# Performance work log

Hardware: AMD Instinct MI355X
Metric: run time of the kernel (lower is better)

## Reference

```python
import jax, jax.numpy as jnp
import numpy as np

B, S, WIDTH, M = 2, 240, 128, 20
PAD = 16


def setup_inputs() -> dict:
    key = jax.random.key(0)
    ks = jax.random.split(key, 10)
    scale = 1.0 / (WIDTH * WIDTH)
    inp = {
        "x": jax.random.normal(ks[0], (B, S, S, 3), jnp.float32),
        "fc0_w": jax.random.normal(ks[1], (5, WIDTH), jnp.float32) * 0.1,
        "fc0_b": jnp.zeros((WIDTH,), jnp.float32),
        # 5 spectral layers, complex weights stored as [..., 2] = (real, imag)
        "spec_w1": jax.random.uniform(ks[2], (5, WIDTH, WIDTH, M, M, 2), jnp.float32) * scale,
        "spec_w2": jax.random.uniform(ks[3], (5, WIDTH, WIDTH, M, M, 2), jnp.float32) * scale,
        # 5 residual 1x1 convs
        "w_w": jax.random.normal(ks[4], (5, WIDTH, WIDTH), jnp.float32) / np.sqrt(WIDTH),
        "w_b": jnp.zeros((5, WIDTH), jnp.float32),
        "fc1_w": jax.random.normal(ks[5], (WIDTH, WIDTH), jnp.float32) / np.sqrt(WIDTH),
        "fc1_b": jnp.zeros((WIDTH,), jnp.float32),
        # 4 heads (u, v, p, T): width->64->1
        "head1_w": jax.random.normal(ks[6], (4, WIDTH, 64), jnp.float32) / np.sqrt(WIDTH),
        "head1_b": jnp.zeros((4, 64), jnp.float32),
        "head2_w": jax.random.normal(ks[7], (4, 64, 1), jnp.float32) / 8.0,
        "head2_b": jnp.zeros((4, 1), jnp.float32),
    }
    return inp


def _spectral_conv(h, w1, w2):
    # h: (B, C, H, W) real; w1, w2: (C_in, C_out, M, M) complex64
    Hh, Ww = h.shape[-2], h.shape[-1]
    ft = jnp.fft.rfft2(h)  # (B, C, H, W//2+1)
    o1 = jnp.einsum('bixy,ioxy->boxy', ft[:, :, :M, :M], w1)
    o2 = jnp.einsum('bixy,ioxy->boxy', ft[:, :, -M:, :M], w2)
    out_ft = jnp.zeros((h.shape[0], w1.shape[1], Hh, Ww // 2 + 1), jnp.complex64)
    out_ft = out_ft.at[:, :, :M, :M].set(o1).at[:, :, -M:, :M].set(o2)
    return jnp.fft.irfft2(out_ft, s=(Hh, Ww))


def reference(x, fc0_w, fc0_b, spec_w1, spec_w2, w_w, w_b, fc1_w, fc1_b,
              head1_w, head1_b, head2_w, head2_b):
    Bn, sx, sy = x.shape[0], x.shape[1], x.shape[2]
    gx = jnp.broadcast_to(jnp.linspace(0.0, 1.0, sx, dtype=x.dtype)[None, :, None, None], (Bn, sx, sy, 1))
    gy = jnp.broadcast_to(jnp.linspace(0.0, 1.0, sy, dtype=x.dtype)[None, None, :, None], (Bn, sx, sy, 1))
    x1 = jnp.concatenate([x, gx, gy], axis=-1)          # (B, S, S, 5)
    h = x1 @ fc0_w + fc0_b                              # lift -> (B, S, S, width)
    h = jnp.transpose(h, (0, 3, 1, 2))                  # (B, width, S, S)
    h = jnp.pad(h, ((0, 0), (0, 0), (0, PAD), (0, PAD)))
    c1 = spec_w1[..., 0] + 1j * spec_w1[..., 1]
    c2 = spec_w2[..., 0] + 1j * spec_w2[..., 1]
    for i in range(5):
        s = _spectral_conv(h, c1[i], c2[i])
        lin = jnp.einsum('bchw,oc->bohw', h, w_w[i]) + w_b[i][None, :, None, None]
        h = s + lin
        if i < 4:
            h = jax.nn.gelu(h, approximate=False)
    h = h[..., :-PAD, :-PAD]
    h = jnp.transpose(h, (0, 2, 3, 1))                  # (B, S, S, width)
    h = jax.nn.gelu(h @ fc1_w + fc1_b, approximate=False)
    h1 = jax.nn.gelu(jnp.einsum('bhwc,kcd->kbhwd', h, head1_w)
                     + head1_b[:, None, None, None, :], approximate=False)
    out = jnp.einsum('kbhwd,kdo->kbhwo', h1, head2_w) + head2_b[:, None, None, None, :]
    return (out[0], out[1], out[2], out[3])  # u, v, p, T each (B, S, S, 1)
```

## Files before the change

kernel.cpp:

```cpp
#include <hip/hip_runtime.h>
#include <math.h>


#define SZ_H   (2ull*256*256*128)
#define O_HA   0ull
#define O_HB   (O_HA + SZ_H)
#define O_G    (O_HB + SZ_H)
#define SZ_G   (2ull*256*20*128*2)
#define O_FTT  (O_G + SZ_G)
#define SZ_FT  (2ull*40*20*128*2)
#define O_OFT  (O_FTT + SZ_FT)
#define O_EY   (O_OFT + SZ_FT)
#define SZ_EY  (256ull*20*2)
#define O_EX   (O_EY + SZ_EY)
#define SZ_EX  (256ull*40*2)
#define O_EXI  (O_EX + SZ_EX)
#define O_WWT  (O_EXI + SZ_EX)
#define SZ_WWT 81920ull
#define O_PART (O_WWT + SZ_WWT)
#define SZ_PART (8ull*204800*2)
#define FC1_B_NEED (O_G + 6356992ull)

static __device__ __forceinline__ float gelu_f(float v) {
    return 0.5f * v * (1.0f + erff(v * 0.70710678118654752f));
}

__global__ void k_prep(const float* __restrict__ w_w, float* __restrict__ ws) {
    int i = blockIdx.x * 256 + threadIdx.x;
    const float STEP = 6.2831853071795864769f / 256.0f;
    if (i < 5120) {
        int ky = i % 20, y = i / 20;
        int t = (ky * y) & 255;
        float th = t * STEP;
        ws[O_EY + 2*(size_t)i]     = cosf(th);
        ws[O_EY + 2*(size_t)i + 1] = -sinf(th);
    } else if (i < 15360) {
        int m = i - 5120; int j = m % 40, x = m / 40;
        int kx = (j < 20) ? j : (216 + j);
        int t = (kx * x) & 255;
        float th = t * STEP;
        ws[O_EX + 2*(size_t)m]     = cosf(th);
        ws[O_EX + 2*(size_t)m + 1] = -sinf(th);
    } else if (i < 25600) {
        int m = i - 15360; int j = m % 40, x = m / 40;
        int kx = (j < 20) ? j : (216 + j);
        int t = (kx * x) & 255;
        float th = t * STEP;
        ws[O_EXI + 2*(size_t)m]     = cosf(th);
        ws[O_EXI + 2*(size_t)m + 1] = sinf(th);
    } else {
        int m = i - 25600;
        if (m < 81920) {
            int l = m >> 14, r = m & 16383;
            int ic = r >> 7, oc = r & 127;
            ws[O_WWT + m] = w_w[(size_t)l*16384 + oc*128 + ic];
        }
    }
}

__global__ __launch_bounds__(256) void k_fc0(const float* __restrict__ xin,
        const float* __restrict__ w, const float* __restrict__ bv,
        float4* __restrict__ H4) {
    size_t e = (size_t)blockIdx.x * 256 + threadIdx.x;
    int c4 = (int)(e & 31) * 4;
    int y = (int)((e >> 5) & 255);
    int x = (int)((e >> 13) & 255);
    int b = (int)(e >> 21);
    float4 h = make_float4(0.f, 0.f, 0.f, 0.f);
    if (x < 240 && y < 240) {
        const float* xp = xin + (((size_t)(b*240 + x))*240 + y)*3;
        float x0 = xp[0], x1 = xp[1], x2 = xp[2];
        float gx = x*(1.0f/239.0f), gy = y*(1.0f/239.0f);
        float4 w0 = *(const float4*)&w[c4];
        float4 w1 = *(const float4*)&w[128 + c4];
        float4 w2 = *(const float4*)&w[256 + c4];
        float4 w3 = *(const float4*)&w[384 + c4];
        float4 w4 = *(const float4*)&w[512 + c4];
        float4 bb = *(const float4*)&bv[c4];
        h.x = bb.x + x0*w0.x + x1*w1.x + x2*w2.x + gx*w3.x + gy*w4.x;
        h.y = bb.y + x0*w0.y + x1*w1.y + x2*w2.y + gx*w3.y + gy*w4.y;
        h.z = bb.z + x0*w0.z + x1*w1.z + x2*w2.z + gx*w3.z + gy*w4.z;
        h.w = bb.w + x0*w0.w + x1*w1.w + x2*w2.w + gx*w3.w + gy*w4.w;
    }
    H4[e] = h;
}

__global__ __launch_bounds__(256) void k_ydft(const float* __restrict__ H,
        const float* __restrict__ Ey, float2* __restrict__ G) {
    int b = blockIdx.x >> 8, x = blockIdx.x & 255;
    int c = threadIdx.x & 127;
    int yq = __builtin_amdgcn_readfirstlane((int)(threadIdx.x >> 7));
    const float* Hrow = H + ((size_t)(b*256 + x)) * 256 * 128;
    float ar[20], ai[20];
    #pragma unroll
    for (int k = 0; k < 20; k++) { ar[k] = 0.f; ai[k] = 0.f; }
    for (int i = 0; i < 128; i++) {
        int y = yq*128 + i;
        float v = Hrow[(size_t)y*128 + c];
        const float* e = Ey + (size_t)y*40;
        #pragma unroll
        for (int k = 0; k < 20; k++) {
            ar[k] = fmaf(v, e[2*k],   ar[k]);
            ai[k] = fmaf(v, e[2*k+1], ai[k]);
        }
    }
    __shared__ float red[20][128][2];
    if (yq == 1) {
        #pragma unroll
        for (int k = 0; k < 20; k++) { red[k][c][0] = ar[k]; red[k][c][1] = ai[k]; }
    }
    __syncthreads();
    if (yq == 0) {
        float2* Gp = G + ((size_t)(b*256 + x))*20*128;
        #pragma unroll
        for (int k = 0; k < 20; k++)
            Gp[k*128 + c] = make_float2(ar[k] + red[k][c][0], ai[k] + red[k][c][1]);
    }
}

__global__ __launch_bounds__(512) void k_xdft(const float2* __restrict__ G,
        const float* __restrict__ Ex, float2* __restrict__ ftT) {
    int t = blockIdx.x;
    int ch = t & 1, jq = (t >> 1) & 1, ky = (t >> 2) % 20, b = t / 80;
    int cl = threadIdx.x & 63;
    int xq = __builtin_amdgcn_readfirstlane((int)(threadIdx.x >> 6));
    int c = ch*64 + cl;
    int j0 = jq * 20;
    float ar[20], ai[20];
    #pragma unroll
    for (int k = 0; k < 20; k++) { ar[k] = 0.f; ai[k] = 0.f; }
    for (int i = 0; i < 32; i++) {
        int x = xq*32 + i;
        float2 g = G[(((size_t)(b*256 + x))*20 + ky)*128 + c];
        const float* e = Ex + (size_t)x*80 + j0*2;
        #pragma unroll
        for (int k = 0; k < 20; k++) {
            float er = e[2*k], ei = e[2*k+1];
            ar[k] = fmaf(g.x, er, fmaf(-g.y, ei, ar[k]));
            ai[k] = fmaf(g.x, ei, fmaf( g.y, er, ai[k]));
        }
    }
    __shared__ float red[4][20][64][2];
    if (xq >= 4) {
        int s = xq - 4;
        #pragma unroll
        for (int k = 0; k < 20; k++) { red[s][k][cl][0] = ar[k]; red[s][k][cl][1] = ai[k]; }
    }
    __syncthreads();
    if (xq < 4) {
        #pragma unroll
        for (int k = 0; k < 20; k++) { ar[k] += red[xq][k][cl][0]; ai[k] += red[xq][k][cl][1]; }
    }
    __syncthreads();
    if (xq == 2 || xq == 3) {
        int s = xq - 2;
        #pragma unroll
        for (int k = 0; k < 20; k++) { red[s][k][cl][0] = ar[k]; red[s][k][cl][1] = ai[k]; }
    }
    __syncthreads();
    if (xq < 2) {
        #pragma unroll
        for (int k = 0; k < 20; k++) { ar[k] += red[xq][k][cl][0]; ai[k] += red[xq][k][cl][1]; }
    }
    __syncthreads();
    if (xq == 1) {
        #pragma unroll
        for (int k = 0; k < 20; k++) { red[0][k][cl][0] = ar[k]; red[0][k][cl][1] = ai[k]; }
    }
    __syncthreads();
    if (xq == 0) {
        #pragma unroll
        for (int k = 0; k < 20; k++) {
            float rr = ar[k] + red[0][k][cl][0];
            float ii = ai[k] + red[0][k][cl][1];
            ftT[((size_t)c*2 + b)*800 + (size_t)(j0 + k)*20 + ky] = make_float2(rr, ii);
        }
    }
}

__global__ __launch_bounds__(448) void k_modemix(const float2* __restrict__ w1,
        const float2* __restrict__ w2, const float2* __restrict__ ftT,
        float2* __restrict__ outp, int ic_per) {
    int bid = blockIdx.x & 255;
    int icq = blockIdx.x >> 8;
    int oc = bid >> 1;
    int mh = bid & 1;
    int tid = threadIdx.x;
    if (tid >= 400) return;
    int wsel = tid / 200;
    int m = mh*200 + (tid % 200);
    int jk = wsel*400 + m;
    const float2* wb = wsel ? w2 : w1;
    int ic0 = icq * ic_per;
    float ar0=0.f, ai0=0.f, ar1=0.f, ai1=0.f;
    #pragma unroll 4
    for (int i = 0; i < ic_per; i++) {
        int ic = ic0 + i;
        float2 wv = wb[((size_t)(ic*128 + oc))*400 + m];
        float2 f0 = ftT[(size_t)ic*1600 + jk];
        float2 f1 = ftT[(size_t)ic*1600 + 800 + jk];
        ar0 = fmaf(f0.x, wv.x, fmaf(-f0.y, wv.y, ar0));
        ai0 = fmaf(f0.x, wv.y, fmaf( f0.y, wv.x, ai0));
        ar1 = fmaf(f1.x, wv.x, fmaf(-f1.y, wv.y, ar1));
        ai1 = fmaf(f1.x, wv.y, fmaf( f1.y, wv.x, ai1));
    }
    float2* o = outp + (size_t)icq * 204800;
    o[(size_t)jk*128 + oc]         = make_float2(ar0, ai0);
    o[(size_t)(800 + jk)*128 + oc] = make_float2(ar1, ai1);
}

__global__ __launch_bounds__(512) void k_modered(const float2* __restrict__ part,
        float2* __restrict__ oft) {
    int i = blockIdx.x * 512 + threadIdx.x;
    if (i >= 204800) return;
    float2 s = part[i];
    #pragma unroll
    for (int q = 1; q < 8; q++) {
        float2 p = part[(size_t)q*204800 + i];
        s.x += p.x; s.y += p.y;
    }
    oft[i] = s;
}

__global__ __launch_bounds__(256) void k_xidft(const float2* __restrict__ oft,
        const float* __restrict__ Exi, float2* __restrict__ T) {
    int b = blockIdx.x >> 7, xq = blockIdx.x & 127;
    int oc = threadIdx.x & 127;
    int xs = __builtin_amdgcn_readfirstlane((int)(threadIdx.x >> 7));
    int x = xq*2 + xs;
    float ar[20], ai[20];
    #pragma unroll
    for (int k = 0; k < 20; k++) { ar[k] = 0.f; ai[k] = 0.f; }
    const float2* ob = oft + (size_t)b*800*128;
    for (int j = 0; j < 40; j++) {
        float er = Exi[(size_t)x*80 + 2*j], ei = Exi[(size_t)x*80 + 2*j + 1];
        #pragma unroll
        for (int k = 0; k < 20; k++) {
            float2 o = ob[(size_t)(j*20 + k)*128 + oc];
            ar[k] = fmaf(o.x, er, fmaf(-o.y, ei, ar[k]));
            ai[k] = fmaf(o.x, ei, fmaf( o.y, er, ai[k]));
        }
    }
    float2* Tp = T + ((size_t)(b*256 + x))*20*128;
    #pragma unroll
    for (int k = 0; k < 20; k++) Tp[k*128 + oc] = make_float2(ar[k], ai[k]);
}

__global__ __launch_bounds__(256) void k_spec_lin(const float* __restrict__ H,
        const float2* __restrict__ T, const float* __restrict__ wwT,
        const float* __restrict__ wb, float* __restrict__ Hout, int do_gelu) {
    int yg = blockIdx.x & 3;
    int x  = (blockIdx.x >> 2) & 255;
    int b  = blockIdx.x >> 10;
    int tid = threadIdx.x;
    int lane = tid & 63;
    int wv = __builtin_amdgcn_readfirstlane(tid >> 6);
    int oc0 = wv * 32;
    int y0 = yg * 64;
    __shared__ float hl[64][129];
    const float* Hbase = H + (((size_t)(b*256 + x))*256 + y0)*128;
    #pragma unroll
    for (int it = 0; it < 8; it++) {
        int i = tid + it*256;
        int pi = i >> 5, c4 = (i & 31)*4;
        float4 v = *(const float4*)&Hbase[(size_t)pi*128 + c4];
        hl[pi][c4] = v.x; hl[pi][c4+1] = v.y; hl[pi][c4+2] = v.z; hl[pi][c4+3] = v.w;
    }
    float csr[20], csi[20];
    {
        int y = y0 + lane;
        #pragma unroll
        for (int k = 0; k < 20; k++) {
            int t = (k * y) & 255;
            float th = t * (6.2831853071795864769f/256.0f);
            float f = (k == 0 ? 1.0f : 2.0f) * (1.0f/65536.0f);
            csr[k] = f * __cosf(th);
            csi[k] = f * __sinf(th);
        }
    }
    __syncthreads();
    float acc[32];
    #pragma unroll
    for (int o = 0; o < 32; o++) acc[o] = 0.f;
    for (int ic = 0; ic < 128; ic++) {
        float t = hl[lane][ic];
        const float* wr = &wwT[(size_t)ic*128 + oc0];
        #pragma unroll
        for (int o4 = 0; o4 < 8; o4++) {
            float4 w = *(const float4*)&wr[o4*4];
            acc[o4*4]   = fmaf(t, w.x, acc[o4*4]);
            acc[o4*4+1] = fmaf(t, w.y, acc[o4*4+1]);
            acc[o4*4+2] = fmaf(t, w.z, acc[o4*4+2]);
            acc[o4*4+3] = fmaf(t, w.w, acc[o4*4+3]);
        }
    }
    const float2* Tp = T + ((size_t)(b*256 + x))*20*128 + oc0;
    for (int k = 0; k < 20; k++) {
        const float2* tr = Tp + (size_t)k*128;
        float cr = csr[k], ci = csi[k];
        #pragma unroll
        for (int o = 0; o < 32; o++) {
            float2 tv = tr[o];
            acc[o] = fmaf(tv.x, cr, fmaf(-tv.y, ci, acc[o]));
        }
    }
    __syncthreads();
    const float* bp = &wb[oc0];
    #pragma unroll
    for (int o = 0; o < 32; o++) {
        float v = acc[o] + bp[o];
        if (do_gelu) v = gelu_f(v);
        hl[lane][oc0 + o] = v;
    }
    __syncthreads();
    float* Obase = Hout + (((size_t)(b*256 + x))*256 + y0)*128;
    #pragma unroll
    for (int it = 0; it < 32; it++) {
        int i = tid + it*256;
        int pi = i >> 7, c = i & 127;
        Obase[(size_t)pi*128 + c] = hl[pi][c];
    }
}

__global__ __launch_bounds__(128) void k_fc1(const float* __restrict__ H,
        const float* __restrict__ fc1_w, const float* __restrict__ fc1_b,
        float* __restrict__ outA, float* __restrict__ outB) {
    int tid = threadIdx.x;
    int lane = tid & 63;
    int wv = __builtin_amdgcn_readfirstlane(tid >> 6);
    int p0 = blockIdx.x * 64;
    __shared__ float hl[64][129];
    #pragma unroll
    for (int it = 0; it < 16; it++) {
        int i = tid + it*128;
        int pi = i >> 5, c4 = (i & 31)*4;
        int p = p0 + pi;
        int bb = p / 57600, r = p % 57600;
        int xx = r / 240, yy = r % 240;
        float4 v = *(const float4*)&H[(((size_t)(bb*256 + xx))*256 + yy)*128 + c4];
        hl[pi][c4] = v.x; hl[pi][c4+1] = v.y; hl[pi][c4+2] = v.z; hl[pi][c4+3] = v.w;
    }
    __syncthreads();
    int oc0 = wv*64;
    float acc[64];
    #pragma unroll
    for (int o = 0; o < 64; o++) acc[o] = 0.f;
    for (int ic = 0; ic < 128; ic++) {
        float t = hl[lane][ic];
        const float* wr = &fc1_w[(size_t)ic*128 + oc0];
        #pragma unroll
        for (int o4 = 0; o4 < 16; o4++) {
            float4 w = *(const float4*)&wr[o4*4];
            acc[o4*4]   = fmaf(t, w.x, acc[o4*4]);
            acc[o4*4+1] = fmaf(t, w.y, acc[o4*4+1]);
            acc[o4*4+2] = fmaf(t, w.z, acc[o4*4+2]);
            acc[o4*4+3] = fmaf(t, w.w, acc[o4*4+3]);
        }
    }
    __syncthreads();
    const float* bp = &fc1_b[oc0];
    #pragma unroll
    for (int o = 0; o < 64; o++) hl[lane][oc0 + o] = gelu_f(acc[o] + bp[o]);
    __syncthreads();
    float* outp = (p0 < 65536) ? (outA + (size_t)p0*128)
                               : (outB + ((size_t)(p0 - 65536))*128);
    #pragma unroll
    for (int it = 0; it < 64; it++) {
        int i = tid + it*128;
        int pi = i >> 7, c = i & 127;
        outp[(size_t)pi*128 + c] = hl[pi][c];
    }
}

__global__ __launch_bounds__(256) void k_heads(const float* __restrict__ inA,
        const float* __restrict__ inB, const float* __restrict__ h1w,
        const float* __restrict__ h1b, const float* __restrict__ h2w,
        const float* __restrict__ h2b, float* __restrict__ out) {
    int tid = threadIdx.x;
    int lane = tid & 63;
    int k = __builtin_amdgcn_readfirstlane(tid >> 6);
    int p0 = blockIdx.x * 64;
    __shared__ float tl[128][65];
    const float* inp = (p0 < 65536) ? (inA + (size_t)p0*128)
                                    : (inB + ((size_t)(p0 - 65536))*128);
    #pragma unroll
    for (int it = 0; it < 8; it++) {
        int i = tid + it*256;
        int pi = i >> 5, c4 = (i & 31)*4;
        float4 v = *(const float4*)&inp[(size_t)pi*128 + c4];
        tl[c4][pi] = v.x; tl[c4+1][pi] = v.y; tl[c4+2][pi] = v.z; tl[c4+3][pi] = v.w;
    }
    __syncthreads();
    float acc[64];
    #pragma unroll
    for (int d = 0; d < 64; d++) acc[d] = 0.f;
    const float* wk = h1w + (size_t)k*8192;
    for (int c = 0; c < 128; c++) {
        float t = tl[c][lane];
        const float* wr = &wk[c*64];
        #pragma unroll
        for (int d4 = 0; d4 < 16; d4++) {
            float4 w = *(const float4*)&wr[d4*4];
            acc[d4*4]   = fmaf(t, w.x, acc[d4*4]);
            acc[d4*4+1] = fmaf(t, w.y, acc[d4*4+1]);
            acc[d4*4+2] = fmaf(t, w.z, acc[d4*4+2]);
            acc[d4*4+3] = fmaf(t, w.w, acc[d4*4+3]);
        }
    }
    const float* b1 = &h1b[k*64];
    const float* w2 = &h2w[k*64];
    float res = 0.f;
    #pragma unroll
    for (int d = 0; d < 64; d++)
        res += gelu_f(acc[d] + b1[d]) * w2[d];
    out[(size_t)k*115200 + p0 + lane] = res + h2b[k];
}

__global__ __launch_bounds__(256) void k_head(const float* __restrict__ H,
        const float* __restrict__ fc1_w, const float* __restrict__ fc1_b,
        const float* __restrict__ h1w, const float* __restrict__ h1b,
        const float* __restrict__ h2w, const float* __restrict__ h2b,
        float* __restrict__ out) {
    int tid = threadIdx.x;
    int p0 = blockIdx.x * 64;
    __shared__ float hl[64][128];
    __shared__ float tl[128][65];
    #pragma unroll
    for (int it = 0; it < 8; it++) {
        int i = tid + it*256;
        int pi = i >> 5, c4 = (i & 31)*4;
        int p = p0 + pi;
        int b = p / 57600, r = p % 57600;
        int xx = r / 240, yy = r % 240;
        *(float4*)&hl[pi][c4] = *(const float4*)&H[(((size_t)(b*256 + xx))*256 + yy)*128 + c4];
    }
    __syncthreads();
    {
        int ocg = tid & 31, pxg = tid >> 5;
        int oc0 = ocg*4, px0 = pxg*8;
        float acc[4][8];
        #pragma unroll
        for (int q = 0; q < 4; q++)
            #pragma unroll
            for (int p = 0; p < 8; p++) acc[q][p] = 0.f;
        for (int icc = 0; icc < 32; icc++) {
            float4 hv[8];
            #pragma unroll
            for (int p = 0; p < 8; p++) hv[p] = *(float4*)&hl[px0 + p][icc*4];
            float4 wA = *(const float4*)&fc1_w[(size_t)(icc*4+0)*128 + oc0];
            float4 wB = *(const float4*)&fc1_w[(size_t)(icc*4+1)*128 + oc0];
            float4 wC = *(const float4*)&fc1_w[(size_t)(icc*4+2)*128 + oc0];
            float4 wD = *(const float4*)&fc1_w[(size_t)(icc*4+3)*128 + oc0];
            #pragma unroll
            for (int p = 0; p < 8; p++) {
                float4 h4 = hv[p];
                acc[0][p] = fmaf(h4.x, wA.x, fmaf(h4.y, wB.x, fmaf(h4.z, wC.x, fmaf(h4.w, wD.x, acc[0][p]))));
                acc[1][p] = fmaf(h4.x, wA.y, fmaf(h4.y, wB.y, fmaf(h4.z, wC.y, fmaf(h4.w, wD.y, acc[1][p]))));
                acc[2][p] = fmaf(h4.x, wA.z, fmaf(h4.y, wB.z, fmaf(h4.z, wC.z, fmaf(h4.w, wD.z, acc[2][p]))));
                acc[3][p] = fmaf(h4.x, wA.w, fmaf(h4.y, wB.w, fmaf(h4.z, wC.w, fmaf(h4.w, wD.w, acc[3][p]))));
            }
        }
        float4 bb = *(const float4*)&fc1_b[oc0];
        float bq[4] = {bb.x, bb.y, bb.z, bb.w};
        #pragma unroll
        for (int q = 0; q < 4; q++)
            #pragma unroll
            for (int p = 0; p < 8; p++)
                tl[oc0 + q][px0 + p] = gelu_f(acc[q][p] + bq[q]);
    }
    __syncthreads();
    {
        int k = tid >> 6, dg = tid & 15, pxg = (tid >> 4) & 3;
        int d0 = dg*4, px0 = pxg*16;
        float acc2[4][16];
        #pragma unroll
        for (int q = 0; q < 4; q++)
            #pragma unroll
            for (int i = 0; i < 16; i++) acc2[q][i] = 0.f;
        const float* wp = h1w + (size_t)k*8192 + d0;
        for (int c = 0; c < 128; c++) {
            float4 w = *(const float4*)&wp[(size_t)c*64];
            #pragma unroll
            for (int i = 0; i < 16; i++) {
                float v = tl[c][px0 + i];
                acc2[0][i] = fmaf(v, w.x, acc2[0][i]);
                acc2[1][i] = fmaf(v, w.y, acc2[1][i]);
                acc2[2][i] = fmaf(v, w.z, acc2[2][i]);
                acc2[3][i] = fmaf(v, w.w, acc2[3][i]);
            }
        }
        float4 b1 = *(const float4*)&h1b[k*64 + d0];
        float4 w2 = *(const float4*)&h2w[k*64 + d0];
        float ob = h2b[k];
        #pragma unroll
        for (int i = 0; i < 16; i++) {
            float u = gelu_f(acc2[0][i] + b1.x) * w2.x
                    + gelu_f(acc2[1][i] + b1.y) * w2.y
                    + gelu_f(acc2[2][i] + b1.z) * w2.z
                    + gelu_f(acc2[3][i] + b1.w) * w2.w;
            u += __shfl_down(u, 8);
            u += __shfl_down(u, 4);
            u += __shfl_down(u, 2);
            u += __shfl_down(u, 1);
            if (dg == 0) out[(size_t)k*115200 + p0 + px0 + i] = u + ob;
        }
    }
}

extern "C" void kernel_launch(void* const* d_in, const int* in_sizes, int n_in,
                              void* d_out, int out_size, void* d_ws, size_t ws_size,
                              hipStream_t stream) {
    const float* x       = (const float*)d_in[0];
    const float* fc0_w   = (const float*)d_in[1];
    const float* fc0_b   = (const float*)d_in[2];
    const float* spec_w1 = (const float*)d_in[3];
    const float* spec_w2 = (const float*)d_in[4];
    const float* w_w     = (const float*)d_in[5];
    const float* w_b     = (const float*)d_in[6];
    const float* fc1_w   = (const float*)d_in[7];
    const float* fc1_b   = (const float*)d_in[8];
    const float* head1_w = (const float*)d_in[9];
    const float* head1_b = (const float*)d_in[10];
    const float* head2_w = (const float*)d_in[11];
    const float* head2_b = (const float*)d_in[12];
    float* ws = (float*)d_ws;
    float* out = (float*)d_out;

    int split      = ws_size >= (size_t)(O_PART + SZ_PART) * 4 ? 1 : 0;
    int head_split = ws_size >= (size_t)FC1_B_NEED * 4 ? 1 : 0;

    k_prep<<<420, 256, 0, stream>>>(w_w, ws);
    k_fc0<<<16384, 256, 0, stream>>>(x, fc0_w, fc0_b, (float4*)(ws + O_HA));

    float* cur = ws + O_HA;
    float* nxt = ws + O_HB;
    float2* G    = (float2*)(ws + O_G);
    float2* ftT  = (float2*)(ws + O_FTT);
    float2* oft  = (float2*)(ws + O_OFT);
    float2* part = (float2*)(ws + O_PART);

    for (int l = 0; l < 5; l++) {
        k_ydft<<<512, 256, 0, stream>>>(cur, ws + O_EY, G);
        k_xdft<<<160, 512, 0, stream>>>(G, ws + O_EX, ftT);
        const float2* w1l = (const float2*)(spec_w1 + (size_t)l*13107200);
        const float2* w2l = (const float2*)(spec_w2 + (size_t)l*13107200);
        if (split) {
            k_modemix<<<2048, 448, 0, stream>>>(w1l, w2l, ftT, part, 16);
            k_modered<<<400, 512, 0, stream>>>(part, oft);
        } else {
            k_modemix<<<256, 448, 0, stream>>>(w1l, w2l, ftT, oft, 128);
        }
        k_xidft<<<256, 256, 0, stream>>>(oft, ws + O_EXI, G);
        k_spec_lin<<<2048, 256, 0, stream>>>(cur, G, ws + O_WWT + (size_t)l*16384,
                                             w_b + l*128, nxt, (l < 4) ? 1 : 0);
        float* t = cur; cur = nxt; nxt = t;
    }
    if (head_split) {
        float* fA = ws + O_HA;
        float* fB = ws + O_G;
        k_fc1<<<1800, 128, 0, stream>>>(cur, fc1_w, fc1_b, fA, fB);
        k_heads<<<1800, 256, 0, stream>>>(fA, fB, head1_w, head1_b,
                                          head2_w, head2_b, out);
    } else {
        k_head<<<1800, 256, 0, stream>>>(cur, fc1_w, fc1_b, head1_w, head1_b,
                                         head2_w, head2_b, out);
    }
}
```

Before: 1.959 ms.

## Retile spectral-linear, fc1 and head kernels; add 4-way mode-mix split fallback

Several independent changes. k_spec_lin now processes 128 y-positions per 512-thread block instead of 64 per 256-thread block, which halves the block count and doubles the tile size. k_fc1 splits its output channels across four waves and writes channel-major (transposed) output directly, dropping the shared-memory staging. k_heads reads that channel-major layout straight from global memory and computes two 64-pixel groups per wave, reusing each weight load. A 4-way partial-sum split is added for mode mixing when the workspace cannot hold the 8-way buffers. The risks are more register pressure in k_heads and uncached strided global loads.

```diff
diff --git a/kernel.cpp b/kernel.cpp
--- a/kernel.cpp
+++ b/kernel.cpp
@@ -18,7 +18,8 @@
 #define O_WWT  (O_EXI + SZ_EX)
 #define SZ_WWT 81920ull
 #define O_PART (O_WWT + SZ_WWT)
-#define SZ_PART (8ull*204800*2)
+#define SZ_PART8 (8ull*204800*2)
+#define SZ_PART4 (4ull*204800*2)
 #define FC1_B_NEED (O_G + 6356992ull)
 
 static __device__ __forceinline__ float gelu_f(float v) {
@@ -210,12 +211,11 @@
 }
 
 __global__ __launch_bounds__(512) void k_modered(const float2* __restrict__ part,
-        float2* __restrict__ oft) {
+        float2* __restrict__ oft, int nq) {
     int i = blockIdx.x * 512 + threadIdx.x;
     if (i >= 204800) return;
     float2 s = part[i];
-    #pragma unroll
-    for (int q = 1; q < 8; q++) {
+    for (int q = 1; q < nq; q++) {
         float2 p = part[(size_t)q*204800 + i];
         s.x += p.x; s.y += p.y;
     }
@@ -246,29 +246,31 @@
     for (int k = 0; k < 20; k++) Tp[k*128 + oc] = make_float2(ar[k], ai[k]);
 }
 
-__global__ __launch_bounds__(256) void k_spec_lin(const float* __restrict__ H,
+__global__ __launch_bounds__(512) void k_spec_lin(const float* __restrict__ H,
         const float2* __restrict__ T, const float* __restrict__ wwT,
         const float* __restrict__ wb, float* __restrict__ Hout, int do_gelu) {
-    int yg = blockIdx.x & 3;
-    int x  = (blockIdx.x >> 2) & 255;
-    int b  = blockIdx.x >> 10;
+    int yg = blockIdx.x & 1;
+    int x  = (blockIdx.x >> 1) & 255;
+    int b  = blockIdx.x >> 9;
     int tid = threadIdx.x;
     int lane = tid & 63;
     int wv = __builtin_amdgcn_readfirstlane(tid >> 6);
-    int oc0 = wv * 32;
-    int y0 = yg * 64;
-    __shared__ float hl[64][129];
+    int oc0 = (wv & 3) * 32;
+    int yh = wv >> 2;
+    int y0 = yg * 128;
+    __shared__ float hl[128][129];
     const float* Hbase = H + (((size_t)(b*256 + x))*256 + y0)*128;
     #pragma unroll
     for (int it = 0; it < 8; it++) {
-        int i = tid + it*256;
+        int i = tid + it*512;
         int pi = i >> 5, c4 = (i & 31)*4;
         float4 v = *(const float4*)&Hbase[(size_t)pi*128 + c4];
         hl[pi][c4] = v.x; hl[pi][c4+1] = v.y; hl[pi][c4+2] = v.z; hl[pi][c4+3] = v.w;
     }
+    int yl = yh*64 + lane;
     float csr[20], csi[20];
     {
-        int y = y0 + lane;
+        int y = y0 + yl;
         #pragma unroll
         for (int k = 0; k < 20; k++) {
             int t = (k * y) & 255;
@@ -283,7 +285,7 @@
     #pragma unroll
     for (int o = 0; o < 32; o++) acc[o] = 0.f;
     for (int ic = 0; ic < 128; ic++) {
-        float t = hl[lane][ic];
+        float t = hl[yl][ic];
         const float* wr = &wwT[(size_t)ic*128 + oc0];
         #pragma unroll
         for (int o4 = 0; o4 < 8; o4++) {
@@ -310,19 +312,19 @@
     for (int o = 0; o < 32; o++) {
         float v = acc[o] + bp[o];
         if (do_gelu) v = gelu_f(v);
-        hl[lane][oc0 + o] = v;
+        hl[yl][oc0 + o] = v;
     }
     __syncthreads();
     float* Obase = Hout + (((size_t)(b*256 + x))*256 + y0)*128;
     #pragma unroll
     for (int it = 0; it < 32; it++) {
-        int i = tid + it*256;
+        int i = tid + it*512;
         int pi = i >> 7, c = i & 127;
         Obase[(size_t)pi*128 + c] = hl[pi][c];
     }
 }
 
-__global__ __launch_bounds__(128) void k_fc1(const float* __restrict__ H,
+__global__ __launch_bounds__(256) void k_fc1(const float* __restrict__ H,
         const float* __restrict__ fc1_w, const float* __restrict__ fc1_b,
         float* __restrict__ outA, float* __restrict__ outB) {
     int tid = threadIdx.x;
@@ -331,8 +333,8 @@
     int p0 = blockIdx.x * 64;
     __shared__ float hl[64][129];
     #pragma unroll
-    for (int it = 0; it < 16; it++) {
-        int i = tid + it*128;
+    for (int it = 0; it < 8; it++) {
+        int i = tid + it*256;
         int pi = i >> 5, c4 = (i & 31)*4;
         int p = p0 + pi;
         int bb = p / 57600, r = p % 57600;
@@ -341,15 +343,15 @@
         hl[pi][c4] = v.x; hl[pi][c4+1] = v.y; hl[pi][c4+2] = v.z; hl[pi][c4+3] = v.w;
     }
     __syncthreads();
-    int oc0 = wv*64;
-    float acc[64];
-    #pragma unroll
-    for (int o = 0; o < 64; o++) acc[o] = 0.f;
+    int oc0 = wv*32;
+    float acc[32];
+    #pragma unroll
+    for (int o = 0; o < 32; o++) acc[o] = 0.f;
     for (int ic = 0; ic < 128; ic++) {
         float t = hl[lane][ic];
         const float* wr = &fc1_w[(size_t)ic*128 + oc0];
         #pragma unroll
-        for (int o4 = 0; o4 < 16; o4++) {
+        for (int o4 = 0; o4 < 8; o4++) {
             float4 w = *(const float4*)&wr[o4*4];
             acc[o4*4]   = fmaf(t, w.x, acc[o4*4]);
             acc[o4*4+1] = fmaf(t, w.y, acc[o4*4+1]);
@@ -357,19 +359,13 @@
             acc[o4*4+3] = fmaf(t, w.w, acc[o4*4+3]);
         }
     }
-    __syncthreads();
+    float* base; size_t pitch; int poff;
+    if (p0 < 65536) { base = outA; pitch = 65536; poff = p0; }
+    else            { base = outB; pitch = 49664; poff = p0 - 65536; }
     const float* bp = &fc1_b[oc0];
     #pragma unroll
-    for (int o = 0; o < 64; o++) hl[lane][oc0 + o] = gelu_f(acc[o] + bp[o]);
-    __syncthreads();
-    float* outp = (p0 < 65536) ? (outA + (size_t)p0*128)
-                               : (outB + ((size_t)(p0 - 65536))*128);
-    #pragma unroll
-    for (int it = 0; it < 64; it++) {
-        int i = tid + it*128;
-        int pi = i >> 7, c = i & 127;
-        outp[(size_t)pi*128 + c] = hl[pi][c];
-    }
+    for (int o = 0; o < 32; o++)
+        base[(size_t)(oc0 + o)*pitch + poff + lane] = gelu_f(acc[o] + bp[o]);
 }
 
 __global__ __launch_bounds__(256) void k_heads(const float* __restrict__ inA,
@@ -379,41 +375,43 @@
     int tid = threadIdx.x;
     int lane = tid & 63;
     int k = __builtin_amdgcn_readfirstlane(tid >> 6);
-    int p0 = blockIdx.x * 64;
-    __shared__ float tl[128][65];
-    const float* inp = (p0 < 65536) ? (inA + (size_t)p0*128)
-                                    : (inB + ((size_t)(p0 - 65536))*128);
-    #pragma unroll
-    for (int it = 0; it < 8; it++) {
-        int i = tid + it*256;
-        int pi = i >> 5, c4 = (i & 31)*4;
-        float4 v = *(const float4*)&inp[(size_t)pi*128 + c4];
-        tl[c4][pi] = v.x; tl[c4+1][pi] = v.y; tl[c4+2][pi] = v.z; tl[c4+3][pi] = v.w;
-    }
-    __syncthreads();
-    float acc[64];
-    #pragma unroll
-    for (int d = 0; d < 64; d++) acc[d] = 0.f;
+    int p0 = blockIdx.x * 128;
+    const float* base; size_t pitch; int poff;
+    if (p0 < 65536) { base = inA; pitch = 65536; poff = p0; }
+    else            { base = inB; pitch = 49664; poff = p0 - 65536; }
+    float acc0[64], acc1[64];
+    #pragma unroll
+    for (int d = 0; d < 64; d++) { acc0[d] = 0.f; acc1[d] = 0.f; }
     const float* wk = h1w + (size_t)k*8192;
     for (int c = 0; c < 128; c++) {
-        float t = tl[c][lane];
+        const float* col = base + (size_t)c*pitch + poff;
+        float t0 = col[lane];
+        float t1 = col[64 + lane];
         const float* wr = &wk[c*64];
         #pragma unroll
         for (int d4 = 0; d4 < 16; d4++) {
             float4 w = *(const float4*)&wr[d4*4];
-            acc[d4*4]   = fmaf(t, w.x, acc[d4*4]);
-            acc[d4*4+1] = fmaf(t, w.y, acc[d4*4+1]);
-            acc[d4*4+2] = fmaf(t, w.z, acc[d4*4+2]);
-            acc[d4*4+3] = fmaf(t, w.w, acc[d4*4+3]);
+            acc0[d4*4]   = fmaf(t0, w.x, acc0[d4*4]);
+            acc0[d4*4+1] = fmaf(t0, w.y, acc0[d4*4+1]);
+            acc0[d4*4+2] = fmaf(t0, w.z, acc0[d4*4+2]);
+            acc0[d4*4+3] = fmaf(t0, w.w, acc0[d4*4+3]);
+            acc1[d4*4]   = fmaf(t1, w.x, acc1[d4*4]);
+            acc1[d4*4+1] = fmaf(t1, w.y, acc1[d4*4+1]);
+            acc1[d4*4+2] = fmaf(t1, w.z, acc1[d4*4+2]);
+            acc1[d4*4+3] = fmaf(t1, w.w, acc1[d4*4+3]);
         }
     }
     const float* b1 = &h1b[k*64];
     const float* w2 = &h2w[k*64];
-    float res = 0.f;
-    #pragma unroll
-    for (int d = 0; d < 64; d++)
-        res += gelu_f(acc[d] + b1[d]) * w2[d];
-    out[(size_t)k*115200 + p0 + lane] = res + h2b[k];
+    float r0 = 0.f, r1 = 0.f;
+    #pragma unroll
+    for (int d = 0; d < 64; d++) {
+        r0 += gelu_f(acc0[d] + b1[d]) * w2[d];
+        r1 += gelu_f(acc1[d] + b1[d]) * w2[d];
+    }
+    float ob = h2b[k];
+    out[(size_t)k*115200 + p0 + lane]      = r0 + ob;
+    out[(size_t)k*115200 + p0 + 64 + lane] = r1 + ob;
 }
 
 __global__ __launch_bounds__(256) void k_head(const float* __restrict__ H,
@@ -526,8 +524,9 @@
     float* ws = (float*)d_ws;
     float* out = (float*)d_out;
 
-    int split      = ws_size >= (size_t)(O_PART + SZ_PART) * 4 ? 1 : 0;
+    int split8     = ws_size >= (size_t)(O_PART + SZ_PART8) * 4 ? 1 : 0;
     int head_split = ws_size >= (size_t)FC1_B_NEED * 4 ? 1 : 0;
+    int split4     = head_split;
 
     k_prep<<<420, 256, 0, stream>>>(w_w, ws);
     k_fc0<<<16384, 256, 0, stream>>>(x, fc0_w, fc0_b, (float4*)(ws + O_HA));
@@ -544,23 +543,26 @@
         k_xdft<<<160, 512, 0, stream>>>(G, ws + O_EX, ftT);
         const float2* w1l = (const float2*)(spec_w1 + (size_t)l*13107200);
         const float2* w2l = (const float2*)(spec_w2 + (size_t)l*13107200);
-        if (split) {
+        if (split8) {
             k_modemix<<<2048, 448, 0, stream>>>(w1l, w2l, ftT, part, 16);
-            k_modered<<<400, 512, 0, stream>>>(part, oft);
+            k_modered<<<400, 512, 0, stream>>>(part, oft, 8);
+        } else if (split4) {
+            k_modemix<<<1024, 448, 0, stream>>>(w1l, w2l, ftT, part, 32);
+            k_modered<<<400, 512, 0, stream>>>(part, oft, 4);
         } else {
             k_modemix<<<256, 448, 0, stream>>>(w1l, w2l, ftT, oft, 128);
         }
         k_xidft<<<256, 256, 0, stream>>>(oft, ws + O_EXI, G);
-        k_spec_lin<<<2048, 256, 0, stream>>>(cur, G, ws + O_WWT + (size_t)l*16384,
+        k_spec_lin<<<1024, 512, 0, stream>>>(cur, G, ws + O_WWT + (size_t)l*16384,
                                              w_b + l*128, nxt, (l < 4) ? 1 : 0);
         float* t = cur; cur = nxt; nxt = t;
     }
     if (head_split) {
         float* fA = ws + O_HA;
         float* fB = ws + O_G;
-        k_fc1<<<1800, 128, 0, stream>>>(cur, fc1_w, fc1_b, fA, fB);
-        k_heads<<<1800, 256, 0, stream>>>(fA, fB, head1_w, head1_b,
-                                          head2_w, head2_b, out);
+        k_fc1<<<1800, 256, 0, stream>>>(cur, fc1_w, fc1_b, fA, fB);
+        k_heads<<<900, 256, 0, stream>>>(fA, fB, head1_w, head1_b,
+                                         head2_w, head2_b, out);
     } else {
         k_head<<<1800, 256, 0, stream>>>(cur, fc1_w, fc1_b, head1_w, head1_b,
                                          head2_w, head2_b, out);
```

New measurement: 2.108 ms. 1.08x slower.
